# Kernel optimization log

Measured on AMD Instinct MI355X. Metric: run time of the kernel, lower is better.

The kernel has to match this reference:

```python
import jax, jax.numpy as jnp
import numpy as np

N_HEAD = 32
N_KV_HEAD = 8
HEAD_DIM = 64
ROPE_THETA = 10000.0


def apply_rope(x):
    # x: [B, H, T, D], interleaved-pair RoPE (rotary_embedding_torch style)
    B, H, T, D = x.shape
    inv_freq = 1.0 / (ROPE_THETA ** (jnp.arange(0, D, 2, dtype=jnp.float32) / D))  # [D/2]
    ang = jnp.arange(T, dtype=jnp.float32)[:, None] * inv_freq[None, :]  # [T, D/2]
    cos = jnp.cos(ang)[None, None].astype(x.dtype)  # [1,1,T,D/2]
    sin = jnp.sin(ang)[None, None].astype(x.dtype)
    xe = x[..., 0::2]
    xo = x[..., 1::2]
    re = xe * cos - xo * sin
    ro = xo * cos + xe * sin
    return jnp.stack([re, ro], axis=-1).reshape(B, H, T, D)


def setup_inputs() -> dict:
    key = jax.random.key(0)
    ks = jax.random.split(key, 5)
    B, T, C = 2, 2048, 2048
    kv_dim = N_KV_HEAD * HEAD_DIM
    s = 0.02
    return {
        "x": jax.random.normal(ks[0], (B, T, C), jnp.float32),
        "wq": jax.random.normal(ks[1], (C, C), jnp.float32) * s,
        "wk": jax.random.normal(ks[2], (C, kv_dim), jnp.float32) * s,
        "wv": jax.random.normal(ks[3], (C, kv_dim), jnp.float32) * s,
        "wo": jax.random.normal(ks[4], (C, C), jnp.float32) * s,
    }


def reference(x, wq, wk, wv, wo):
    B, T, C = x.shape
    hd = HEAD_DIM
    q = (x @ wq).reshape(B, T, N_HEAD, hd).transpose(0, 2, 1, 3)      # [B,H,T,d]
    k = (x @ wk).reshape(B, T, N_KV_HEAD, hd).transpose(0, 2, 1, 3)   # [B,Hkv,T,d]
    v = (x @ wv).reshape(B, T, N_KV_HEAD, hd).transpose(0, 2, 1, 3)
    q = apply_rope(q)
    k = apply_rope(k)
    rep = N_HEAD // N_KV_HEAD
    k = jnp.repeat(k, rep, axis=1)  # repeat_interleave over head dim
    v = jnp.repeat(v, rep, axis=1)
    att = jnp.einsum('bhqd,bhkd->bhqk', q, k) * (1.0 / np.sqrt(hd))
    causal = jnp.tril(jnp.ones((T, T), dtype=bool))
    att = jnp.where(causal[None, None], att, jnp.finfo(att.dtype).min)
    att = jax.nn.softmax(att, axis=-1)
    y = jnp.einsum('bhqk,bhkd->bhqd', att, v)
    y = y.transpose(0, 2, 1, 3).reshape(B, T, C)
    return y @ wo
```

## Files before the change

### kernel.cpp

```cpp
#include <hip/hip_runtime.h>
#include <hip/hip_bf16.h>
#include <cstdint>
#include <cstddef>


using bf16 = __hip_bfloat16;
using f32x4  = __attribute__((ext_vector_type(4))) float;
using f32x16 = __attribute__((ext_vector_type(16))) float;
using short8 = __attribute__((ext_vector_type(8))) short;
using u32x4  = __attribute__((ext_vector_type(4))) unsigned int;

typedef __attribute__((address_space(1))) const void* gp1_t;
typedef __attribute__((address_space(3))) void*       lp3_t;

#define GLOAD_LDS16(g, l)                                                     \
  __builtin_amdgcn_global_load_lds((gp1_t)(const void*)(g), (lp3_t)(void*)(l), 16, 0, 0)

#define MFMA16(a, b, c) __builtin_amdgcn_mfma_f32_16x16x32_bf16(a, b, c, 0, 0, 0)
#define MFMA32(a, b, c) __builtin_amdgcn_mfma_f32_32x32x16_bf16(a, b, c, 0, 0, 0)

static constexpr int Bd  = 2;
static constexpr int Td  = 2048;
static constexpr int Cd  = 2048;
static constexpr int NH  = 32;
static constexpr int NKV = 8;
static constexpr int HD  = 64;
static constexpr int Md  = Bd * Td;

__device__ inline float bf2f(unsigned short u) {
  union { unsigned int i; float f; } v; v.i = ((unsigned int)u) << 16; return v.f;
}
__device__ inline unsigned short f2bfbits(float f) {
  union { float f; unsigned int u; } v; v.f = f;
  unsigned int r = v.u + 0x7fffu + ((v.u >> 16) & 1u);
  return (unsigned short)(r >> 16);
}
__device__ inline unsigned int pkbf(float a, float b) {
  unsigned int r;
  asm("v_cvt_pk_bf16_f32 %0, %1, %2" : "=v"(r) : "v"(a), "v"(b));
  return r;
}
__device__ inline void plswapf(float& a, float& b) {
  asm("v_permlane32_swap_b32 %0, %1" : "+v"(a), "+v"(b));
}
__device__ inline void plswapu(unsigned int& a, unsigned int& b) {
  asm("v_permlane32_swap_b32 %0, %1" : "+v"(a), "+v"(b));
}
__device__ inline float hmax16(const f32x16& v) {
  float a0 = fmaxf(v[0], v[1]),   a1 = fmaxf(v[2], v[3]);
  float a2 = fmaxf(v[4], v[5]),   a3 = fmaxf(v[6], v[7]);
  float a4 = fmaxf(v[8], v[9]),   a5 = fmaxf(v[10], v[11]);
  float a6 = fmaxf(v[12], v[13]), a7 = fmaxf(v[14], v[15]);
  float b0 = fmaxf(a0, a1), b1 = fmaxf(a2, a3);
  float b2 = fmaxf(a4, a5), b3 = fmaxf(a6, a7);
  return fmaxf(fmaxf(b0, b1), fmaxf(b2, b3));
}
__device__ inline float hsum16(const f32x16& v) {
  float a0 = v[0]+v[1],   a1 = v[2]+v[3],   a2 = v[4]+v[5],   a3 = v[6]+v[7];
  float a4 = v[8]+v[9],   a5 = v[10]+v[11], a6 = v[12]+v[13], a7 = v[14]+v[15];
  float b0 = a0+a1, b1 = a2+a3, b2 = a4+a5, b3 = a6+a7;
  return (b0+b1)+(b2+b3);
}

__global__ __launch_bounds__(256) void prep1_kernel(const float* __restrict__ x,
                                                    const float* __restrict__ wq,
                                                    const float* __restrict__ wk,
                                                    const float* __restrict__ wv,
                                                    bf16* __restrict__ xb,
                                                    bf16* __restrict__ w1) {
  __shared__ float tile[32][33];
  int bid = blockIdx.x, tid = threadIdx.x;
  if (bid < 8192) {
    int i = bid * 256 + tid;
    float4 v = ((const float4*)x)[i];
    ushort4 o;
    o.x = f2bfbits(v.x); o.y = f2bfbits(v.y); o.z = f2bfbits(v.z); o.w = f2bfbits(v.w);
    ((ushort4*)xb)[i] = o;
    return;
  }
  const float* in; bf16* out; int Cc, bx, by;
  if (bid < 12288)      { int l = bid - 8192;  in = wq; out = w1;                        Cc = 2048; bx = l & 63; by = l >> 6; }
  else if (bid < 13312) { int l = bid - 12288; in = wk; out = w1 + (size_t)2048 * 2048;  Cc = 512;  bx = l & 15; by = l >> 4; }
  else                  { int l = bid - 13312; in = wv; out = w1 + (size_t)2560 * 2048;  Cc = 512;  bx = l & 15; by = l >> 4; }
  int tx = tid & 31, ty = tid >> 5;
  int col = bx * 32 + tx;
#pragma unroll
  for (int i = 0; i < 4; ++i) {
    int row = by * 32 + ty + i * 8;
    tile[ty + i * 8][tx] = in[(size_t)row * Cc + col];
  }
  __syncthreads();
#pragma unroll
  for (int i = 0; i < 4; ++i) {
    int orow = bx * 32 + ty + i * 8;
    int ocol = by * 32 + tx;
    out[(size_t)orow * 2048 + ocol] = __float2bfloat16(tile[tx][ty + i * 8]);
  }
}

__global__ __launch_bounds__(256) void transpose_f2b(const float* __restrict__ in,
                                                     bf16* __restrict__ out,
                                                     int R, int Cc) {
  __shared__ float tile[32][33];
  int tx = threadIdx.x & 31, ty = threadIdx.x >> 5;
  int bx = blockIdx.x, by = blockIdx.y;
  int col = bx * 32 + tx;
#pragma unroll
  for (int i = 0; i < 4; ++i) {
    int row = by * 32 + ty + i * 8;
    tile[ty + i * 8][tx] = in[(size_t)row * Cc + col];
  }
  __syncthreads();
#pragma unroll
  for (int i = 0; i < 4; ++i) {
    int orow = bx * 32 + ty + i * 8;
    int ocol = by * 32 + tx;
    out[(size_t)orow * R + ocol] = __float2bfloat16(tile[tx][ty + i * 8]);
  }
}

template <int MODE>
__global__ __launch_bounds__(512, 2) void gemm_bf16(const bf16* __restrict__ A,
                                                    const bf16* __restrict__ Bt,
                                                    void* __restrict__ Cp,
                                                    int M, int N, int K) {
  __shared__ __align__(16) char lds[131072];
  int tid = threadIdx.x;
  int w = tid >> 6, lane = tid & 63;
  int lr = lane & 15, lg = lane >> 4;
  int m0 = blockIdx.x * 256, n0 = blockIdx.y * 256;
  int wr = w >> 2, wc = w & 3;
  f32x4 acc[8][4] = {};

  size_t Kb = (size_t)K * 2;
  int c8 = lane & 7, r8 = lane >> 3;
  const char* Asrc = (const char*)A + (size_t)(m0 + w * 8 + r8) * Kb + ((c8 ^ r8) << 4);
  const char* Bsrc = (const char*)Bt + (size_t)(n0 + w * 8 + r8) * Kb + ((c8 ^ r8) << 4);
  char* AldsW = lds + w * 1024;
  char* BldsW = lds + 65536 + w * 1024;

#define GSTAGE(kt, bb) do {                                                   \
    _Pragma("unroll")                                                         \
    for (int j = 0; j < 4; ++j) {                                             \
      GLOAD_LDS16(Asrc + (size_t)j * 64 * Kb + (size_t)(kt) * 2,              \
                  AldsW + (bb) * 32768 + j * 8192);                           \
      GLOAD_LDS16(Bsrc + (size_t)j * 64 * Kb + (size_t)(kt) * 2,              \
                  BldsW + (bb) * 32768 + j * 8192);                           \
    }                                                                         \
  } while (0)

  int nkt = K >> 6;
  GSTAGE(0, 0);
  asm volatile("s_waitcnt vmcnt(0)" ::: "memory");
  __builtin_amdgcn_s_barrier();

  for (int t = 0; t < nkt; ++t) {
    int cur = t & 1;
    const char* Ab = lds + cur * 32768;
    const char* Bb = lds + 65536 + cur * 32768;
    short8 af[4][2], bfr[4][2];

    if (t + 1 < nkt) GSTAGE((t + 1) << 6, cur ^ 1);
#pragma unroll
    for (int kk = 0; kk < 2; ++kk) {
      int cb = (((kk << 2) | lg) ^ (lr & 7)) << 4;
#pragma unroll
      for (int f = 0; f < 4; ++f) {
        af[f][kk]  = *(const short8*)(Ab + (size_t)(wr * 128 + f * 16 + lr) * 128 + cb);
        bfr[f][kk] = *(const short8*)(Bb + (size_t)(wc * 64 + f * 16 + lr) * 128 + cb);
      }
    }
    __builtin_amdgcn_s_barrier();
    asm volatile("s_waitcnt lgkmcnt(0)" ::: "memory");
    __builtin_amdgcn_sched_barrier(0);
    __builtin_amdgcn_s_setprio(1);
#pragma unroll
    for (int f = 0; f < 4; ++f)
#pragma unroll
      for (int g = 0; g < 2; ++g)
#pragma unroll
        for (int kk = 0; kk < 2; ++kk)
          acc[f][g] = MFMA16(af[f][kk], bfr[g][kk], acc[f][g]);
    __builtin_amdgcn_s_setprio(0);
    __builtin_amdgcn_sched_barrier(0);
    __builtin_amdgcn_s_barrier();

    __builtin_amdgcn_s_setprio(1);
#pragma unroll
    for (int f = 0; f < 4; ++f)
#pragma unroll
      for (int g = 2; g < 4; ++g)
#pragma unroll
        for (int kk = 0; kk < 2; ++kk)
          acc[f][g] = MFMA16(af[f][kk], bfr[g][kk], acc[f][g]);
    __builtin_amdgcn_s_setprio(0);
    __builtin_amdgcn_sched_barrier(0);
    __builtin_amdgcn_s_barrier();

#pragma unroll
    for (int kk = 0; kk < 2; ++kk) {
      int cb = (((kk << 2) | lg) ^ (lr & 7)) << 4;
#pragma unroll
      for (int f = 0; f < 4; ++f)
        af[f][kk] = *(const short8*)(Ab + (size_t)(wr * 128 + 64 + f * 16 + lr) * 128 + cb);
    }
    __builtin_amdgcn_s_barrier();
    asm volatile("s_waitcnt lgkmcnt(0)" ::: "memory");
    __builtin_amdgcn_sched_barrier(0);
    __builtin_amdgcn_s_setprio(1);
#pragma unroll
    for (int f = 0; f < 4; ++f)
#pragma unroll
      for (int g = 0; g < 2; ++g)
#pragma unroll
        for (int kk = 0; kk < 2; ++kk)
          acc[4 + f][g] = MFMA16(af[f][kk], bfr[g][kk], acc[4 + f][g]);
    __builtin_amdgcn_s_setprio(0);
    __builtin_amdgcn_sched_barrier(0);
    __builtin_amdgcn_s_barrier();

    __builtin_amdgcn_s_setprio(1);
#pragma unroll
    for (int f = 0; f < 4; ++f)
#pragma unroll
      for (int g = 2; g < 4; ++g)
#pragma unroll
        for (int kk = 0; kk < 2; ++kk)
          acc[4 + f][g] = MFMA16(af[f][kk], bfr[g][kk], acc[4 + f][g]);
    __builtin_amdgcn_s_setprio(0);
    __builtin_amdgcn_sched_barrier(0);
    asm volatile("s_waitcnt vmcnt(0)" ::: "memory");
    __builtin_amdgcn_s_barrier();
  }
#undef GSTAGE

  bf16* Qb  = (bf16*)Cp;
  bf16* Kb2 = Qb + (size_t)Bd * NH * Td * HD;
  bf16* Vtb = Kb2 + (size_t)Bd * NKV * Td * HD;

  if (MODE == 3 && n0 >= 2560) {
    int b  = m0 >> 11;
    int tg = (m0 & 2047) + wr * 128;
    int h  = (n0 - 2560 + wc * 64) >> 6;
    char* tb = lds + w * 16384;
#pragma unroll
    for (int i = 0; i < 8; ++i)
#pragma unroll
      for (int j = 0; j < 4; ++j)
#pragma unroll
        for (int r = 0; r < 4; r += 2) {
          int d  = j * 16 + lr;
          int tt = i * 16 + lg * 4 + r;
          unsigned int pk = pkbf(acc[i][j][r], acc[i][j][r + 1]);
          *(unsigned int*)(tb + (((size_t)d * 256 + tt * 2) ^ ((d & 7) << 4))) = pk;
        }
    asm volatile("s_waitcnt lgkmcnt(0)" ::: "memory");
    __builtin_amdgcn_sched_barrier(0);
    char* Vdst = (char*)Vtb + (((size_t)(b * NKV + h) * 64) * Td + tg) * 2;
#pragma unroll
    for (int p = 0; p < 16; ++p) {
      int d  = p * 4 + (lane >> 4);
      int tc = lane & 15;
      u32x4 v = *(const u32x4*)(tb + (((size_t)d * 256 + tc * 16) ^ ((d & 7) << 4)));
      *(u32x4*)(Vdst + (size_t)d * Td * 2 + tc * 16) = v;
    }
    return;
  }

  if (MODE == 3) {
    const float RC = -0.41524101186092029f;
    float sc = (n0 < 2048) ? 0.18033688011112042f : 1.0f;
    int odd = lane & 1;
#pragma unroll
    for (int j = 0; j < 4; ++j) {
      int ncol = n0 + wc * 64 + j * 16 + lr;
      int d  = ncol & 63;
      float inv = __builtin_amdgcn_exp2f((float)(d >> 1) * RC);
#pragma unroll
      for (int i = 0; i < 8; ++i) {
#pragma unroll
        for (int r = 0; r < 4; ++r) {
          int mrow = m0 + wr * 128 + i * 16 + lg * 4 + r;
          int t = mrow & 2047;
          float v = acc[i][j][r];
          float p = __shfl_xor(v, 1);
          float rev = (float)t * inv * 0.15915494309189535f;
          rev = rev - floorf(rev);
          float s = __builtin_amdgcn_sinf(rev);
          float c = __builtin_amdgcn_cosf(rev);
          float res = odd ? (v * c + p * s) : (v * c - p * s);
          res *= sc;
          int b = mrow >> 11;
          if (n0 < 2048) {
            int h = ncol >> 6;
            Qb[(((size_t)b * NH + h) * Td + t) * HD + d] = __float2bfloat16(res);
          } else {
            int h = (ncol - 2048) >> 6;
            Kb2[(((size_t)b * NKV + h) * Td + t) * HD + d] = __float2bfloat16(res);
          }
        }
      }
    }
    return;
  }

#pragma unroll
  for (int i = 0; i < 8; ++i)
#pragma unroll
    for (int j = 0; j < 4; ++j)
#pragma unroll
      for (int r = 0; r < 4; ++r) {
        int mrow = m0 + wr * 128 + i * 16 + lg * 4 + r;
        int ncol = n0 + wc * 64 + j * 16 + lr;
        ((float*)Cp)[(size_t)mrow * N + ncol] = acc[i][j][r];
      }
}

__global__ __launch_bounds__(512, 4) void attn_kernel(const bf16* __restrict__ Q,
                                                      const bf16* __restrict__ K,
                                                      const bf16* __restrict__ Vt,
                                                      bf16* __restrict__ Y) {
  __shared__ __align__(16) char lds[2 * 16384];
  int tid = threadIdx.x, w = tid >> 6, lane = tid & 63;
  int lq = lane & 31;
  int H  = lane >> 5;
  int qb = 7 - (int)blockIdx.y;
  int bh = blockIdx.x;
  int b = bh >> 5, h = bh & 31, kvh = h >> 2;
  int q0w = qb * 256 + w * 32;
  int qg  = q0w + lq;
  int tmax = qb * 4 + (w >> 1);
  int Nt   = qb * 4 + 4;

  const bf16* Qp = Q + (((size_t)b * NH + h) * Td) * HD;
  const char* Kg = (const char*)(K + (((size_t)b * NKV + kvh) * Td) * HD);
  const char* Vg = (const char*)(Vt + (((size_t)b * NKV + kvh) * HD) * Td);

  short8 qf[4];
#pragma unroll
  for (int ck = 0; ck < 4; ++ck)
    qf[ck] = *(const short8*)(Qp + (size_t)qg * HD + ck * 16 + H * 8);

  int srow   = lane >> 3;
  int scol16 = ((lane & 7) ^ srow) << 4;
  const char* Ksrc0 = Kg + (size_t)(w * 8 + srow) * 128 + scol16;
  const char* Vsrc0 = Vg + (size_t)(w * 8 + srow) * 4096 + scol16;
  char* KldsW[2] = { lds + w * 1024,          lds + 16384 + w * 1024 };
  char* VldsW[2] = { lds + 8192 + w * 1024,   lds + 24576 + w * 1024 };

#define STAGE_KV(tt, bb) do {                                                 \
    GLOAD_LDS16(Ksrc0 + (size_t)(tt) * 64 * 128, KldsW[bb]);                  \
    GLOAD_LDS16(Vsrc0 + (size_t)(tt) * 128,      VldsW[bb]);                  \
  } while (0)

  f32x16 acc0 = {}, acc1 = {};
  float m = -3e38f, l = 0.0f;
  int swz = (lq & 7) << 4;
  int rb0 = lq * 128, rb1 = (32 + lq) * 128;

  STAGE_KV(0, 0);
  asm volatile("s_waitcnt vmcnt(0)" ::: "memory");
  __syncthreads();

  for (int t = 0; t < Nt; ++t) {
    int cur = t & 1;
    if (t + 1 < Nt) STAGE_KV(t + 1, cur ^ 1);
    if (t <= tmax) {
      const char* Kl = lds + cur * 16384;
      const char* Vl = Kl + 8192;
      f32x16 s0 = {}, s1 = {};
      __builtin_amdgcn_s_setprio(1);
#pragma unroll
      for (int ck = 0; ck < 4; ++ck) {
        int c = (H * 16 + ck * 32) ^ swz;
        short8 kf0 = *(const short8*)(Kl + rb0 + c);
        short8 kf1 = *(const short8*)(Kl + rb1 + c);
        s0 = MFMA32(kf0, qf[ck], s0);
        s1 = MFMA32(kf1, qf[ck], s1);
      }
      __builtin_amdgcn_s_setprio(0);
      if (t == tmax) {
        int kvb = t * 64;
#pragma unroll
        for (int rr = 0; rr < 16; ++rr) {
          int krel = (rr & 3) + 8 * (rr >> 2) + 4 * H;
          if (kvb + krel > qg)      s0[rr] = -3e38f;
          if (kvb + 32 + krel > qg) s1[rr] = -3e38f;
        }
      }
      float mx = fmaxf(hmax16(s0), hmax16(s1));
      {
        float mb = mx;
        asm("" : "+v"(mb));
        plswapf(mx, mb);
        mx = fmaxf(mx, mb);
      }
      if (__any(mx > m + 8.0f)) {
        float mn = fmaxf(m, mx);
        float al = __builtin_amdgcn_exp2f(m - mn);
        m = mn;
        l *= al;
#pragma unroll
        for (int rr = 0; rr < 16; ++rr) { acc0[rr] *= al; acc1[rr] *= al; }
      }
#pragma unroll
      for (int rr = 0; rr < 16; ++rr) {
        s0[rr] = __builtin_amdgcn_exp2f(s0[rr] - m);
        s1[rr] = __builtin_amdgcn_exp2f(s1[rr] - m);
      }
      float ps = hsum16(s0) + hsum16(s1);
      {
        float pb = ps;
        asm("" : "+v"(pb));
        plswapf(ps, pb);
        ps += pb;
      }
      l += ps;
      short8 pf[4];
#pragma unroll
      for (int tt = 0; tt < 2; ++tt) {
        const f32x16& sv = tt ? s1 : s0;
#pragma unroll
        for (int a2 = 0; a2 < 2; ++a2) {
          unsigned int A0 = pkbf(sv[8*a2 + 0], sv[8*a2 + 1]);
          unsigned int A1 = pkbf(sv[8*a2 + 2], sv[8*a2 + 3]);
          unsigned int B0 = pkbf(sv[8*a2 + 4], sv[8*a2 + 5]);
          unsigned int B1 = pkbf(sv[8*a2 + 6], sv[8*a2 + 7]);
          plswapu(A0, B0);
          plswapu(A1, B1);
          u32x4 t4;
          t4[0] = A0; t4[1] = A1; t4[2] = B0; t4[3] = B1;
          pf[2*tt + a2] = __builtin_bit_cast(short8, t4);
        }
      }
      __builtin_amdgcn_s_setprio(1);
#pragma unroll
      for (int ks = 0; ks < 4; ++ks) {
        int c = (H * 16 + ks * 32) ^ swz;
        short8 vf0 = *(const short8*)(Vl + rb0 + c);
        short8 vf1 = *(const short8*)(Vl + rb1 + c);
        acc0 = MFMA32(vf0, pf[ks], acc0);
        acc1 = MFMA32(vf1, pf[ks], acc1);
      }
      __builtin_amdgcn_s_setprio(0);
    }
    asm volatile("s_waitcnt vmcnt(0)" ::: "memory");
    __syncthreads();
  }
#undef STAGE_KV

  float rn = 1.0f / l;
  bf16* Yp = Y + ((size_t)b * Td + qg) * Cd + h * HD;
#pragma unroll
  for (int rr = 0; rr < 16; rr += 2) {
    int d = (rr & 3) + 8 * (rr >> 2) + 4 * H;
    unsigned int w0 = pkbf(acc0[rr] * rn, acc0[rr + 1] * rn);
    unsigned int w1 = pkbf(acc1[rr] * rn, acc1[rr + 1] * rn);
    *(unsigned int*)(Yp + d)      = w0;
    *(unsigned int*)(Yp + 32 + d) = w1;
  }
}

extern "C" void kernel_launch(void* const* d_in, const int* in_sizes, int n_in,
                              void* d_out, int out_size, void* d_ws, size_t ws_size,
                              hipStream_t stream) {
  const float* x  = (const float*)d_in[0];
  const float* wq = (const float*)d_in[1];
  const float* wk = (const float*)d_in[2];
  const float* wv = (const float*)d_in[3];
  const float* wo = (const float*)d_in[4];

  char* ws = (char*)d_ws;
  const size_t o_xb = 0;
  const size_t o_w1 = o_xb + (size_t)Md * Cd * 2;
  const size_t o_Q  = o_w1 + (size_t)3072 * Cd * 2;
  const size_t o_K  = o_Q + (size_t)Bd * NH * Td * HD * 2;
  const size_t o_V  = o_K + (size_t)Bd * NKV * Td * HD * 2;

  bf16* xb  = (bf16*)(ws + o_xb);
  bf16* w1  = (bf16*)(ws + o_w1);
  bf16* Qb  = (bf16*)(ws + o_Q);
  bf16* Kb  = (bf16*)(ws + o_K);
  bf16* Vtb = (bf16*)(ws + o_V);
  bf16* yb  = xb;

  prep1_kernel<<<dim3(14336), dim3(256), 0, stream>>>(x, wq, wk, wv, xb, w1);
  gemm_bf16<3><<<dim3(Md / 256, 3072 / 256), dim3(512), 0, stream>>>(xb, w1, Qb, Md, 3072, Cd);
  transpose_f2b<<<dim3(Cd / 32, Cd / 32), dim3(256), 0, stream>>>(wo, w1, Cd, Cd);
  attn_kernel<<<dim3(Bd * NH, 8), dim3(512), 0, stream>>>(Qb, Kb, Vtb, yb);
  gemm_bf16<2><<<dim3(Md / 256, Cd / 256), dim3(512), 0, stream>>>(yb, w1, d_out, Md, Cd, Cd);
}
```

Measured before the change: 212.0 us.

## Add dedicated 128x128-tile output projection GEMM for better CU occupancy

Splits the templated GEMM into a QKV-specific kernel and a new output-projection kernel. The new kernel uses 128x128 tiles, 256-thread blocks and a double-buffered LDS pipeline. For the 4096x2048x2048 output GEMM this gives 512 blocks instead of 128, so the 256 CUs are better filled. The cost is less data reuse per tile and more total global traffic.

Result: faster. 193.7 us (median of 2 runs) (-8.7%).

```diff
diff --git a/kernel.cpp b/kernel.cpp
--- a/kernel.cpp
+++ b/kernel.cpp
@@ -119,11 +119,10 @@
   }
 }
 
-template <int MODE>
-__global__ __launch_bounds__(512, 2) void gemm_bf16(const bf16* __restrict__ A,
-                                                    const bf16* __restrict__ Bt,
-                                                    void* __restrict__ Cp,
-                                                    int M, int N, int K) {
+__global__ __launch_bounds__(512, 2) void gemm_qkv(const bf16* __restrict__ A,
+                                                   const bf16* __restrict__ Bt,
+                                                   void* __restrict__ Cp,
+                                                   int M, int N, int K) {
   __shared__ __align__(16) char lds[131072];
   int tid = threadIdx.x;
   int w = tid >> 6, lane = tid & 63;
@@ -238,7 +237,7 @@
   bf16* Kb2 = Qb + (size_t)Bd * NH * Td * HD;
   bf16* Vtb = Kb2 + (size_t)Bd * NKV * Td * HD;
 
-  if (MODE == 3 && n0 >= 2560) {
+  if (n0 >= 2560) {
     int b  = m0 >> 11;
     int tg = (m0 & 2047) + wr * 128;
     int h  = (n0 - 2560 + wc * 64) >> 6;
@@ -267,52 +266,121 @@
     return;
   }
 
-  if (MODE == 3) {
-    const float RC = -0.41524101186092029f;
-    float sc = (n0 < 2048) ? 0.18033688011112042f : 1.0f;
-    int odd = lane & 1;
-#pragma unroll
-    for (int j = 0; j < 4; ++j) {
-      int ncol = n0 + wc * 64 + j * 16 + lr;
-      int d  = ncol & 63;
-      float inv = __builtin_amdgcn_exp2f((float)(d >> 1) * RC);
-#pragma unroll
-      for (int i = 0; i < 8; ++i) {
-#pragma unroll
-        for (int r = 0; r < 4; ++r) {
-          int mrow = m0 + wr * 128 + i * 16 + lg * 4 + r;
-          int t = mrow & 2047;
-          float v = acc[i][j][r];
-          float p = __shfl_xor(v, 1);
-          float rev = (float)t * inv * 0.15915494309189535f;
-          rev = rev - floorf(rev);
-          float s = __builtin_amdgcn_sinf(rev);
-          float c = __builtin_amdgcn_cosf(rev);
-          float res = odd ? (v * c + p * s) : (v * c - p * s);
-          res *= sc;
-          int b = mrow >> 11;
-          if (n0 < 2048) {
-            int h = ncol >> 6;
-            Qb[(((size_t)b * NH + h) * Td + t) * HD + d] = __float2bfloat16(res);
-          } else {
-            int h = (ncol - 2048) >> 6;
-            Kb2[(((size_t)b * NKV + h) * Td + t) * HD + d] = __float2bfloat16(res);
-          }
-        }
-      }
-    }
-    return;
-  }
-
-#pragma unroll
-  for (int i = 0; i < 8; ++i)
-#pragma unroll
-    for (int j = 0; j < 4; ++j)
+  const float RC = -0.41524101186092029f;
+  float sc = (n0 < 2048) ? 0.18033688011112042f : 1.0f;
+  int odd = lane & 1;
+#pragma unroll
+  for (int j = 0; j < 4; ++j) {
+    int ncol = n0 + wc * 64 + j * 16 + lr;
+    int d  = ncol & 63;
+    float inv = __builtin_amdgcn_exp2f((float)(d >> 1) * RC);
+#pragma unroll
+    for (int i = 0; i < 8; ++i) {
 #pragma unroll
       for (int r = 0; r < 4; ++r) {
         int mrow = m0 + wr * 128 + i * 16 + lg * 4 + r;
+        int t = mrow & 2047;
+        float v = acc[i][j][r];
+        float p = __shfl_xor(v, 1);
+        float rev = (float)t * inv * 0.15915494309189535f;
+        rev = rev - floorf(rev);
+        float s = __builtin_amdgcn_sinf(rev);
+        float c = __builtin_amdgcn_cosf(rev);
+        float res = odd ? (v * c + p * s) : (v * c - p * s);
+        res *= sc;
+        int b = mrow >> 11;
+        if (n0 < 2048) {
+          int h = ncol >> 6;
+          Qb[(((size_t)b * NH + h) * Td + t) * HD + d] = __float2bfloat16(res);
+        } else {
+          int h = (ncol - 2048) >> 6;
+          Kb2[(((size_t)b * NKV + h) * Td + t) * HD + d] = __float2bfloat16(res);
+        }
+      }
+    }
+  }
+}
+
+__global__ __launch_bounds__(256, 2) void gemm_out(const bf16* __restrict__ A,
+                                                   const bf16* __restrict__ Bt,
+                                                   float* __restrict__ Cp,
+                                                   int M, int N, int K) {
+  __shared__ __align__(16) bf16 Al[2][128 * 64];
+  __shared__ __align__(16) bf16 Bl[2][128 * 64];
+  int tid = threadIdx.x;
+  int w = tid >> 6, lane = tid & 63;
+  int lr = lane & 15, lg = lane >> 4;
+  int m0 = blockIdx.x * 128, n0 = blockIdx.y * 128;
+  int wr = w >> 1, wc = w & 1;
+  f32x4 acc[4][4] = {};
+
+  size_t Kb = (size_t)K * 2;
+  int c8 = lane & 7, r8 = lane >> 3;
+  const char* Asrc = (const char*)A + (size_t)(m0 + w * 8 + r8) * Kb + ((c8 ^ r8) << 4);
+  const char* Bsrc = (const char*)Bt + (size_t)(n0 + w * 8 + r8) * Kb + ((c8 ^ r8) << 4);
+
+#define GSTAGE(kt, bb) do {                                                   \
+    char* ald = (char*)&Al[bb][0] + w * 1024;                                 \
+    char* bld = (char*)&Bl[bb][0] + w * 1024;                                 \
+    _Pragma("unroll")                                                         \
+    for (int j = 0; j < 4; ++j) {                                             \
+      GLOAD_LDS16(Asrc + (size_t)j * 32 * Kb + (size_t)(kt) * 2, ald + j * 4096); \
+      GLOAD_LDS16(Bsrc + (size_t)j * 32 * Kb + (size_t)(kt) * 2, bld + j * 4096); \
+    }                                                                         \
+  } while (0)
+
+  int nkt = K >> 6;
+  GSTAGE(0, 0);
+  asm volatile("s_waitcnt vmcnt(0)" ::: "memory");
+  __builtin_amdgcn_s_barrier();
+  __builtin_amdgcn_sched_barrier(0);
+
+  for (int t = 0; t < nkt; ++t) {
+    int cur = t & 1;
+    if (t + 1 < nkt) {
+      GSTAGE((t + 1) << 6, cur ^ 1);
+      asm volatile("s_waitcnt vmcnt(8)" ::: "memory");
+    } else {
+      asm volatile("s_waitcnt vmcnt(0)" ::: "memory");
+    }
+    __builtin_amdgcn_s_barrier();
+    __builtin_amdgcn_sched_barrier(0);
+    const char* Ab = (const char*)&Al[cur][0];
+    const char* Bb = (const char*)&Bl[cur][0];
+    __builtin_amdgcn_s_setprio(1);
+#pragma unroll
+    for (int kk = 0; kk < 2; ++kk) {
+      short8 af[4], bfr[4];
+#pragma unroll
+      for (int f = 0; f < 4; ++f) {
+        int ra = wr * 64 + f * 16 + lr;
+        int rb = wc * 64 + f * 16 + lr;
+        int cb = (((kk << 2) | lg) ^ (lr & 7)) << 4;
+        af[f]  = *(const short8*)(Ab + (size_t)ra * 128 + cb);
+        bfr[f] = *(const short8*)(Bb + (size_t)rb * 128 + cb);
+      }
+#pragma unroll
+      for (int i = 0; i < 4; ++i)
+#pragma unroll
+        for (int j = 0; j < 4; ++j)
+          acc[i][j] = MFMA16(af[i], bfr[j], acc[i][j]);
+    }
+    __builtin_amdgcn_s_setprio(0);
+    asm volatile("s_waitcnt lgkmcnt(0)" ::: "memory");
+    __builtin_amdgcn_sched_barrier(0);
+    __builtin_amdgcn_s_barrier();
+  }
+#undef GSTAGE
+
+#pragma unroll
+  for (int i = 0; i < 4; ++i)
+#pragma unroll
+    for (int j = 0; j < 4; ++j)
+#pragma unroll
+      for (int r = 0; r < 4; ++r) {
+        int mrow = m0 + wr * 64 + i * 16 + lg * 4 + r;
         int ncol = n0 + wc * 64 + j * 16 + lr;
-        ((float*)Cp)[(size_t)mrow * N + ncol] = acc[i][j][r];
+        Cp[(size_t)mrow * N + ncol] = acc[i][j][r];
       }
 }
 
@@ -485,8 +553,8 @@
   bf16* yb  = xb;
 
   prep1_kernel<<<dim3(14336), dim3(256), 0, stream>>>(x, wq, wk, wv, xb, w1);
-  gemm_bf16<3><<<dim3(Md / 256, 3072 / 256), dim3(512), 0, stream>>>(xb, w1, Qb, Md, 3072, Cd);
+  gemm_qkv<<<dim3(Md / 256, 3072 / 256), dim3(512), 0, stream>>>(xb, w1, Qb, Md, 3072, Cd);
   transpose_f2b<<<dim3(Cd / 32, Cd / 32), dim3(256), 0, stream>>>(wo, w1, Cd, Cd);
   attn_kernel<<<dim3(Bd * NH, 8), dim3(512), 0, stream>>>(Qb, Kb, Vtb, yb);
-  gemm_bf16<2><<<dim3(Md / 256, Cd / 256), dim3(512), 0, stream>>>(yb, w1, d_out, Md, Cd, Cd);
-}
+  gemm_out<<<dim3(Md / 128, Cd / 128), dim3(256), 0, stream>>>(yb, w1, (float*)d_out, Md, Cd, Cd);
+}
```
